# Optimization experiments

Hardware: AMD Instinct MI355X
Metric: run time of the kernel (lower is better)

Reference implementation:

```python
import jax, jax.numpy as jnp
import numpy as np

GAMMA = 2.0                  # n2n_gamma
WAVELET_WEIGHT = 0.05
THRESHOLD = 50.0 / 255.0     # wavelet_threshold normalized
LEVELS = 3


def conv_model(x, weight):
    # Stand-in denoising network: 1->1 channel 3x3 SAME conv.
    return jax.lax.conv_general_dilated(
        x, weight, window_strides=(1, 1), padding='SAME',
        dimension_numbers=('NCHW', 'OIHW', 'NCHW'))


def generate_subimages_checkerboard(noisy):
    # 2x2 checkerboard: (even,even) and (odd,odd), bilinearly upsampled back
    # to (H, W). jax.image.resize 'linear' uses half-pixel centers, matching
    # torch F.interpolate(mode='bilinear', align_corners=False).
    B, C, H, W = noisy.shape  # H, W assumed even (512)
    p0 = noisy[:, :, 0::2, 0::2]
    p3 = noisy[:, :, 1::2, 1::2]
    g1 = jax.image.resize(p0, (B, C, H, W), method='linear')
    g2 = jax.image.resize(p3, (B, C, H, W), method='linear')
    return g1, g2


def haar_level(x):
    # One level of batched 2D Haar DWT on x: [B, H, W] (H, W even).
    a = x[:, 0::2, 0::2]
    b = x[:, 0::2, 1::2]
    c = x[:, 1::2, 0::2]
    d = x[:, 1::2, 1::2]
    ll = (a + b + c + d) * 0.5
    lh = (a - b + c - d) * 0.5  # horizontal detail
    hl = (a + b - c - d) * 0.5  # vertical detail
    hh = (a - b - c + d) * 0.5  # diagonal detail
    return ll, (lh, hl, hh)


def wavelet_sparsity_loss(pred):
    # pred: [B, C, H, W]; only channel 0 is used (as in the original).
    # L1(c, soft_threshold(c, t)) == mean(min(|c|, t)) since the target is
    # detached; pywt's coeffs[1] is the COARSEST detail level, with
    # threshold t/2^(level_idx-1) and weight 1/level_idx, so the finest
    # decomposition step j maps to level_idx = LEVELS - j + 1.
    x = pred[:, 0]  # [B, H, W]
    total = jnp.asarray(0.0, dtype=x.dtype)
    cur = x
    for j in range(1, LEVELS + 1):  # j=1 finest
        cur, (h, v, d) = haar_level(cur)
        level_idx = LEVELS - j + 1
        thr = THRESHOLD / (2.0 ** (level_idx - 1))
        w = 1.0 / level_idx
        lvl = (jnp.mean(jnp.minimum(jnp.abs(h), thr)) +
               jnp.mean(jnp.minimum(jnp.abs(v), thr)) +
               jnp.mean(jnp.minimum(jnp.abs(d), thr))) / 3.0
        total = total + w * lvl
    return total


def setup_inputs() -> dict:
    key = jax.random.key(0)
    k1, k2 = jax.random.split(key)
    noisy_input = jax.random.uniform(k1, (32, 1, 512, 512), dtype=jnp.float32)
    weight = jax.random.normal(k2, (1, 1, 3, 3), dtype=jnp.float32) * (1.0 / 3.0)
    return {"noisy_input": noisy_input, "weight": weight}


def reference(noisy_input, weight):
    g1, g2 = generate_subimages_checkerboard(noisy_input)
    out = jnp.clip(conv_model(g1, weight), 0.0, 1.0)
    rec = jnp.mean((out - g2) ** 2)
    reg = jnp.mean((out - g1) ** 2)
    n2n_total = rec + GAMMA * reg
    # Original detaches pred to numpy for the wavelet prior -> no gradient.
    wavelet = jax.lax.stop_gradient(wavelet_sparsity_loss(out))
    return n2n_total + WAVELET_WEIGHT * wavelet
```

## Files before the change

### kernel.cpp

```cpp
#include <hip/hip_runtime.h>

namespace {

constexpr int   IMG = 512;
constexpr float THR = 50.0f / 255.0f;
constexpr int   NBLOCKS = (IMG / 32) * (IMG / 32) * 32;

constexpr double N_PIX = 32.0 * 512.0 * 512.0;
constexpr double N_L1  = 32.0 * 256.0 * 256.0;
constexpr double N_L2  = 32.0 * 128.0 * 128.0;
constexpr double N_L3  = 32.0 * 64.0 * 64.0;
constexpr double C_REC = 1.0 / N_PIX;
constexpr double C_REG = 2.0 / N_PIX;
constexpr double C_W1  = 0.05 / (9.0 * N_L1);
constexpr double C_W2  = 0.05 / (6.0 * N_L2);
constexpr double C_W3  = 0.05 / (3.0 * N_L3);

__global__ __launch_bounds__(256) void n2n_wavelet_kernel(
    const float* __restrict__ noisy,
    const float* __restrict__ weight,
    double* __restrict__ partial) {
  __shared__ float sP0[18][20];
  __shared__ float sP3[18][20];
  __shared__ float sG1[34][36];
  __shared__ float sOut[32][36];
  __shared__ float sLL1[16][18];
  __shared__ float sLL2[8][10];
  __shared__ float sRed[4][5];

  const int t  = threadIdx.x;
  const int tx = blockIdx.x;
  const int ty = blockIdx.y;
  const int b  = blockIdx.z;
  const float* img = noisy + (size_t)b * IMG * IMG;

  const int py0 = 16 * ty - 1;
  const int px0 = 16 * tx - 1;

  float wk[9];
#pragma unroll
  for (int i = 0; i < 9; ++i) wk[i] = weight[i];

  {
    const int r = t >> 4, c = t & 15;
    auto stage = [&](int rr, int cc) {
      int gr = py0 + rr; gr = gr < 0 ? 0 : (gr > 255 ? 255 : gr);
      int gc = px0 + cc; gc = gc < 0 ? 0 : (gc > 255 ? 255 : gc);
      sP0[rr][cc] = img[(gr * 2) * IMG + gc * 2];
      sP3[rr][cc] = img[(gr * 2 + 1) * IMG + gc * 2 + 1];
    };
    stage(r, c);
    if (c < 2) stage(r, c + 16);
    if (r < 2) stage(r + 16, c);
    if (r < 2 && c < 2) stage(r + 16, c + 16);
  }
  __syncthreads();

  const int gyb0 = 32 * ty, gxb0 = 32 * tx;

  for (int q = t; q < 289; q += 256) {
    const int n = q / 17;
    const int m = q - n * 17;
    const float a  = sP0[n][m],     bb = sP0[n][m + 1];
    const float cc = sP0[n + 1][m], dd = sP0[n + 1][m + 1];
    const float xt0 = 0.75f * a + 0.25f * bb;
    const float xt1 = 0.25f * a + 0.75f * bb;
    const float xb0 = 0.75f * cc + 0.25f * dd;
    const float xb1 = 0.25f * cc + 0.75f * dd;
    float v00 = 0.75f * xt0 + 0.25f * xb0;
    float v01 = 0.75f * xt1 + 0.25f * xb1;
    float v10 = 0.25f * xt0 + 0.75f * xb0;
    float v11 = 0.25f * xt1 + 0.75f * xb1;
    const int gyt = gyb0 - 1 + 2 * n, gxl = gxb0 - 1 + 2 * m;
    const bool vt = (unsigned)gyt < (unsigned)IMG, vb = (unsigned)(gyt + 1) < (unsigned)IMG;
    const bool vl = (unsigned)gxl < (unsigned)IMG, vr = (unsigned)(gxl + 1) < (unsigned)IMG;
    v00 = (vt && vl) ? v00 : 0.0f;  v01 = (vt && vr) ? v01 : 0.0f;
    v10 = (vb && vl) ? v10 : 0.0f;  v11 = (vb && vr) ? v11 : 0.0f;
    *(float2*)&sG1[2 * n][2 * m]     = make_float2(v00, v01);
    *(float2*)&sG1[2 * n + 1][2 * m] = make_float2(v10, v11);
  }
  __syncthreads();

  float rec = 0.0f, rgg = 0.0f;
  {
    const int row  = t >> 3;
    const int col0 = (t & 7) << 2;
    float a0 = 0, a1 = 0, a2 = 0, a3 = 0;
    float g1c0 = 0, g1c1 = 0, g1c2 = 0, g1c3 = 0;
#pragma unroll
    for (int u = 0; u < 3; ++u) {
      const float4 q4 = *(const float4*)&sG1[row + u][col0];
      const float2 e2 = *(const float2*)&sG1[row + u][col0 + 4];
      const float w0 = wk[3 * u], w1 = wk[3 * u + 1], w2 = wk[3 * u + 2];
      a0 += w0 * q4.x + w1 * q4.y + w2 * q4.z;
      a1 += w0 * q4.y + w1 * q4.z + w2 * q4.w;
      a2 += w0 * q4.z + w1 * q4.w + w2 * e2.x;
      a3 += w0 * q4.w + w1 * e2.x + w2 * e2.y;
      if (u == 1) { g1c0 = q4.y; g1c1 = q4.z; g1c2 = q4.w; g1c3 = e2.x; }
    }
    const float o0 = fminf(fmaxf(a0, 0.0f), 1.0f);
    const float o1 = fminf(fmaxf(a1, 0.0f), 1.0f);
    const float o2 = fminf(fmaxf(a2, 0.0f), 1.0f);
    const float o3 = fminf(fmaxf(a3, 0.0f), 1.0f);
    *(float4*)&sOut[row][col0] = make_float4(o0, o1, o2, o3);

    const int   r0l = (row >> 1) + (row & 1);
    const float wyt = (row & 1) ? 0.75f : 0.25f;
    const float wyb = 1.0f - wyt;
    const int   c0l = col0 >> 1;
    const float2 t01 = *(const float2*)&sP3[r0l][c0l];
    const float2 t23 = *(const float2*)&sP3[r0l][c0l + 2];
    const float2 b01 = *(const float2*)&sP3[r0l + 1][c0l];
    const float2 b23 = *(const float2*)&sP3[r0l + 1][c0l + 2];
    const float xt0 = 0.25f * t01.x + 0.75f * t01.y;
    const float xt1 = 0.75f * t01.y + 0.25f * t23.x;
    const float xt2 = 0.25f * t01.y + 0.75f * t23.x;
    const float xt3 = 0.75f * t23.x + 0.25f * t23.y;
    const float xb0 = 0.25f * b01.x + 0.75f * b01.y;
    const float xb1 = 0.75f * b01.y + 0.25f * b23.x;
    const float xb2 = 0.25f * b01.y + 0.75f * b23.x;
    const float xb3 = 0.75f * b23.x + 0.25f * b23.y;
    const float g20 = wyt * xt0 + wyb * xb0;
    const float g21 = wyt * xt1 + wyb * xb1;
    const float g22 = wyt * xt2 + wyb * xb2;
    const float g23 = wyt * xt3 + wyb * xb3;

    float d;
    d = o0 - g20; rec += d * d;   d = o1 - g21; rec += d * d;
    d = o2 - g22; rec += d * d;   d = o3 - g23; rec += d * d;
    d = o0 - g1c0; rgg += d * d;  d = o1 - g1c1; rgg += d * d;
    d = o2 - g1c2; rgg += d * d;  d = o3 - g1c3; rgg += d * d;
  }
  __syncthreads();

  float w1a = 0.0f, w2a = 0.0f, w3a = 0.0f;
  {
    const int i = t >> 4, j = t & 15;
    const float2 top = *(const float2*)&sOut[2 * i][2 * j];
    const float2 bot = *(const float2*)&sOut[2 * i + 1][2 * j];
    const float aa = top.x, bb = top.y, cc = bot.x, dd = bot.y;
    sLL1[i][j] = (aa + bb + cc + dd) * 0.5f;
    const float lh = (aa - bb + cc - dd) * 0.5f;
    const float hl = (aa + bb - cc - dd) * 0.5f;
    const float hh = (aa - bb - cc + dd) * 0.5f;
    const float th = THR * 0.25f;
    w1a = fminf(fabsf(lh), th) + fminf(fabsf(hl), th) + fminf(fabsf(hh), th);
  }
  __syncthreads();
  if (t < 64) {
    const int i = t >> 3, j = t & 7;
    const float2 top = *(const float2*)&sLL1[2 * i][2 * j];
    const float2 bot = *(const float2*)&sLL1[2 * i + 1][2 * j];
    const float aa = top.x, bb = top.y, cc = bot.x, dd = bot.y;
    sLL2[i][j] = (aa + bb + cc + dd) * 0.5f;
    const float lh = (aa - bb + cc - dd) * 0.5f;
    const float hl = (aa + bb - cc - dd) * 0.5f;
    const float hh = (aa - bb - cc + dd) * 0.5f;
    const float th = THR * 0.5f;
    w2a = fminf(fabsf(lh), th) + fminf(fabsf(hl), th) + fminf(fabsf(hh), th);
  }
  __syncthreads();
  if (t < 16) {
    const int i = t >> 2, j = t & 3;
    const float2 top = *(const float2*)&sLL2[2 * i][2 * j];
    const float2 bot = *(const float2*)&sLL2[2 * i + 1][2 * j];
    const float aa = top.x, bb = top.y, cc = bot.x, dd = bot.y;
    const float lh = (aa - bb + cc - dd) * 0.5f;
    const float hl = (aa + bb - cc - dd) * 0.5f;
    const float hh = (aa - bb - cc + dd) * 0.5f;
    w3a = fminf(fabsf(lh), THR) + fminf(fabsf(hl), THR) + fminf(fabsf(hh), THR);
  }

  float vals[5] = {rec, rgg, w1a, w2a, w3a};
#pragma unroll
  for (int v = 0; v < 5; ++v) {
    float x = vals[v];
#pragma unroll
    for (int off = 32; off > 0; off >>= 1) x += __shfl_down(x, off);
    vals[v] = x;
  }
  const int wave = t >> 6, lane = t & 63;
  if (lane == 0) {
#pragma unroll
    for (int v = 0; v < 5; ++v) sRed[wave][v] = vals[v];
  }
  __syncthreads();
  if (t == 0) {
    double s[5];
#pragma unroll
    for (int v = 0; v < 5; ++v)
      s[v] = (double)(sRed[0][v] + sRed[1][v] + sRed[2][v] + sRed[3][v]);
    const double contrib =
        C_REC * s[0] + C_REG * s[1] + C_W1 * s[2] + C_W2 * s[3] + C_W3 * s[4];
    const int bid = (blockIdx.z * gridDim.y + blockIdx.y) * gridDim.x + blockIdx.x;
    partial[bid] = contrib;
  }
}

__global__ __launch_bounds__(256) void finalize_kernel(
    const double* __restrict__ partial, float* __restrict__ out) {
  __shared__ double sRed[4];
  const int t = threadIdx.x;
  double s = 0.0;
  for (int i = t; i < NBLOCKS; i += 256) s += partial[i];
#pragma unroll
  for (int off = 32; off > 0; off >>= 1) s += __shfl_down(s, off);
  if ((t & 63) == 0) sRed[t >> 6] = s;
  __syncthreads();
  if (t == 0) out[0] = (float)(sRed[0] + sRed[1] + sRed[2] + sRed[3]);
}

}

extern "C" void kernel_launch(void* const* d_in, const int* in_sizes, int n_in,
                              void* d_out, int out_size, void* d_ws, size_t ws_size,
                              hipStream_t stream) {
  const float* noisy  = (const float*)d_in[0];
  const float* weight = (const float*)d_in[1];
  double* partial = (double*)d_ws;
  float* out = (float*)d_out;

  dim3 grid(IMG / 32, IMG / 32, 32);
  hipLaunchKernelGGL(n2n_wavelet_kernel, grid, dim3(256), 0, stream, noisy, weight, partial);
  hipLaunchKernelGGL(finalize_kernel, dim3(1), dim3(256), 0, stream, partial, out);
}
```

Measured before the change: 104.2 us.

## Replace shared-memory tiles with per-wave register strip pipeline and shuffles

Each wave now processes an 8-row strip across the full 512-pixel width, with each lane handling 8 columns. Upsampling, conv, loss terms and all three Haar levels are computed in registers, with neighbours exchanged by lane shuffles. This removes the shared-memory staging, the block barriers and the redundant halo loads of the 32x32 tile scheme, and reads rows as coalesced float4 loads. The cost is higher register pressure (launch bounds of 2 blocks per SM), fully unrolled code, and more partials (one per wave) for the finalize kernel to sum.

```diff
diff --git a/kernel.cpp b/kernel.cpp
--- a/kernel.cpp
+++ b/kernel.cpp
@@ -2,9 +2,12 @@
 
 namespace {
 
-constexpr int   IMG = 512;
+constexpr int IMG = 512;
+constexpr int S = 8;
+constexpr int NSTRIPS = IMG / S;
+constexpr int NWAVES = 32 * NSTRIPS;
+constexpr int NBLK = NWAVES / 4;
 constexpr float THR = 50.0f / 255.0f;
-constexpr int   NBLOCKS = (IMG / 32) * (IMG / 32) * 32;
 
 constexpr double N_PIX = 32.0 * 512.0 * 512.0;
 constexpr double N_L1  = 32.0 * 256.0 * 256.0;
@@ -16,184 +19,201 @@
 constexpr double C_W2  = 0.05 / (6.0 * N_L2);
 constexpr double C_W3  = 0.05 / (3.0 * N_L3);
 
-__global__ __launch_bounds__(256) void n2n_wavelet_kernel(
+struct F4 { float v[4]; };
+struct F8 { float v[8]; };
+struct Row { F8 g; float gl, gr; };
+
+__device__ __forceinline__ F4 load_even_cols(const float* rowp) {
+  const float4 lo = *(const float4*)rowp;
+  const float4 hi = *(const float4*)(rowp + 4);
+  F4 r; r.v[0] = lo.x; r.v[1] = lo.z; r.v[2] = hi.x; r.v[3] = hi.z; return r;
+}
+__device__ __forceinline__ F4 load_odd_cols(const float* rowp) {
+  const float4 lo = *(const float4*)rowp;
+  const float4 hi = *(const float4*)(rowp + 4);
+  F4 r; r.v[0] = lo.y; r.v[1] = lo.w; r.v[2] = hi.y; r.v[3] = hi.w; return r;
+}
+
+__device__ __forceinline__ F8 hblend(const F4& p, int lane) {
+  float left  = __shfl_up(p.v[3], 1);
+  float right = __shfl_down(p.v[0], 1);
+  if (lane == 0)  left  = p.v[0];
+  if (lane == 63) right = p.v[3];
+  F8 h;
+  h.v[0] = 0.25f*left   + 0.75f*p.v[0];
+  h.v[1] = 0.75f*p.v[0] + 0.25f*p.v[1];
+  h.v[2] = 0.25f*p.v[0] + 0.75f*p.v[1];
+  h.v[3] = 0.75f*p.v[1] + 0.25f*p.v[2];
+  h.v[4] = 0.25f*p.v[1] + 0.75f*p.v[2];
+  h.v[5] = 0.75f*p.v[2] + 0.25f*p.v[3];
+  h.v[6] = 0.25f*p.v[2] + 0.75f*p.v[3];
+  h.v[7] = 0.75f*p.v[3] + 0.25f*right;
+  return h;
+}
+
+__device__ __forceinline__ Row vblend(const F8& a, const F8& b, float wa, float wb, int lane) {
+  Row r;
+#pragma unroll
+  for (int c = 0; c < 8; ++c) r.g.v[c] = wa*a.v[c] + wb*b.v[c];
+  const float gl = __shfl_up(r.g.v[7], 1);
+  const float gr = __shfl_down(r.g.v[0], 1);
+  r.gl = (lane == 0)  ? 0.0f : gl;
+  r.gr = (lane == 63) ? 0.0f : gr;
+  return r;
+}
+
+__device__ __forceinline__ void conv_acc(const Row& r, const float* wk3, F8& acc) {
+#pragma unroll
+  for (int c = 0; c < 8; ++c) {
+    const float gm1 = (c == 0) ? r.gl : r.g.v[c-1];
+    const float gp1 = (c == 7) ? r.gr : r.g.v[c+1];
+    acc.v[c] += wk3[0]*gm1 + wk3[1]*r.g.v[c] + wk3[2]*gp1;
+  }
+}
+
+__device__ __forceinline__ F8 conv3(const Row& r0, const Row& r1, const Row& r2,
+                                    const float* wk) {
+  F8 o;
+#pragma unroll
+  for (int c = 0; c < 8; ++c) o.v[c] = 0.0f;
+  conv_acc(r0, wk + 0, o);
+  conv_acc(r1, wk + 3, o);
+  conv_acc(r2, wk + 6, o);
+#pragma unroll
+  for (int c = 0; c < 8; ++c) o.v[c] = fminf(fmaxf(o.v[c], 0.0f), 1.0f);
+  return o;
+}
+
+__device__ __forceinline__ F4 haarL1(const F8& e, const F8& o, float thr, float& acc) {
+  F4 ll;
+#pragma unroll
+  for (int c = 0; c < 4; ++c) {
+    const float a = e.v[2*c], b = e.v[2*c+1], cc = o.v[2*c], d = o.v[2*c+1];
+    ll.v[c] = (a + b + cc + d) * 0.5f;
+    const float lh = (a - b + cc - d) * 0.5f;
+    const float hl = (a + b - cc - d) * 0.5f;
+    const float hh = (a - b - cc + d) * 0.5f;
+    acc += fminf(fabsf(lh), thr) + fminf(fabsf(hl), thr) + fminf(fabsf(hh), thr);
+  }
+  return ll;
+}
+
+__device__ __forceinline__ float haar1pair(float a, float b, float cc, float d,
+                                           float thr, float& acc) {
+  const float lh = (a - b + cc - d) * 0.5f;
+  const float hl = (a + b - cc - d) * 0.5f;
+  const float hh = (a - b - cc + d) * 0.5f;
+  acc += fminf(fabsf(lh), thr) + fminf(fabsf(hl), thr) + fminf(fabsf(hh), thr);
+  return (a + b + cc + d) * 0.5f;
+}
+
+__global__ __launch_bounds__(256, 2) void n2n_wavelet_kernel(
     const float* __restrict__ noisy,
     const float* __restrict__ weight,
     double* __restrict__ partial) {
-  __shared__ float sP0[18][20];
-  __shared__ float sP3[18][20];
-  __shared__ float sG1[34][36];
-  __shared__ float sOut[32][36];
-  __shared__ float sLL1[16][18];
-  __shared__ float sLL2[8][10];
-  __shared__ float sRed[4][5];
-
-  const int t  = threadIdx.x;
-  const int tx = blockIdx.x;
-  const int ty = blockIdx.y;
-  const int b  = blockIdx.z;
-  const float* img = noisy + (size_t)b * IMG * IMG;
-
-  const int py0 = 16 * ty - 1;
-  const int px0 = 16 * tx - 1;
+  const int t = threadIdx.x;
+  const int lane = t & 63;
+  const int gwid = blockIdx.x * 4 + (t >> 6);
+  const int strip = gwid & (NSTRIPS - 1);
+  const int b = gwid >> 6;
+  const float* base = noisy + (size_t)b * IMG * IMG + lane * 8;
+
+  const int y0 = strip * S;
+  const int k0 = y0 >> 1;
+  const bool lastStrip = (y0 == IMG - S);
 
   float wk[9];
 #pragma unroll
   for (int i = 0; i < 9; ++i) wk[i] = weight[i];
 
-  {
-    const int r = t >> 4, c = t & 15;
-    auto stage = [&](int rr, int cc) {
-      int gr = py0 + rr; gr = gr < 0 ? 0 : (gr > 255 ? 255 : gr);
-      int gc = px0 + cc; gc = gc < 0 ? 0 : (gc > 255 ? 255 : gc);
-      sP0[rr][cc] = img[(gr * 2) * IMG + gc * 2];
-      sP3[rr][cc] = img[(gr * 2 + 1) * IMG + gc * 2 + 1];
-    };
-    stage(r, c);
-    if (c < 2) stage(r, c + 16);
-    if (r < 2) stage(r + 16, c);
-    if (r < 2 && c < 2) stage(r + 16, c + 16);
-  }
-  __syncthreads();
-
-  const int gyb0 = 32 * ty, gxb0 = 32 * tx;
-
-  for (int q = t; q < 289; q += 256) {
-    const int n = q / 17;
-    const int m = q - n * 17;
-    const float a  = sP0[n][m],     bb = sP0[n][m + 1];
-    const float cc = sP0[n + 1][m], dd = sP0[n + 1][m + 1];
-    const float xt0 = 0.75f * a + 0.25f * bb;
-    const float xt1 = 0.25f * a + 0.75f * bb;
-    const float xb0 = 0.75f * cc + 0.25f * dd;
-    const float xb1 = 0.25f * cc + 0.75f * dd;
-    float v00 = 0.75f * xt0 + 0.25f * xb0;
-    float v01 = 0.75f * xt1 + 0.25f * xb1;
-    float v10 = 0.25f * xt0 + 0.75f * xb0;
-    float v11 = 0.25f * xt1 + 0.75f * xb1;
-    const int gyt = gyb0 - 1 + 2 * n, gxl = gxb0 - 1 + 2 * m;
-    const bool vt = (unsigned)gyt < (unsigned)IMG, vb = (unsigned)(gyt + 1) < (unsigned)IMG;
-    const bool vl = (unsigned)gxl < (unsigned)IMG, vr = (unsigned)(gxl + 1) < (unsigned)IMG;
-    v00 = (vt && vl) ? v00 : 0.0f;  v01 = (vt && vr) ? v01 : 0.0f;
-    v10 = (vb && vl) ? v10 : 0.0f;  v11 = (vb && vr) ? v11 : 0.0f;
-    *(float2*)&sG1[2 * n][2 * m]     = make_float2(v00, v01);
-    *(float2*)&sG1[2 * n + 1][2 * m] = make_float2(v10, v11);
-  }
-  __syncthreads();
-
-  float rec = 0.0f, rgg = 0.0f;
-  {
-    const int row  = t >> 3;
-    const int col0 = (t & 7) << 2;
-    float a0 = 0, a1 = 0, a2 = 0, a3 = 0;
-    float g1c0 = 0, g1c1 = 0, g1c2 = 0, g1c3 = 0;
-#pragma unroll
-    for (int u = 0; u < 3; ++u) {
-      const float4 q4 = *(const float4*)&sG1[row + u][col0];
-      const float2 e2 = *(const float2*)&sG1[row + u][col0 + 4];
-      const float w0 = wk[3 * u], w1 = wk[3 * u + 1], w2 = wk[3 * u + 2];
-      a0 += w0 * q4.x + w1 * q4.y + w2 * q4.z;
-      a1 += w0 * q4.y + w1 * q4.z + w2 * q4.w;
-      a2 += w0 * q4.z + w1 * q4.w + w2 * e2.x;
-      a3 += w0 * q4.w + w1 * e2.x + w2 * e2.y;
-      if (u == 1) { g1c0 = q4.y; g1c1 = q4.z; g1c2 = q4.w; g1c3 = e2.x; }
-    }
-    const float o0 = fminf(fmaxf(a0, 0.0f), 1.0f);
-    const float o1 = fminf(fmaxf(a1, 0.0f), 1.0f);
-    const float o2 = fminf(fmaxf(a2, 0.0f), 1.0f);
-    const float o3 = fminf(fmaxf(a3, 0.0f), 1.0f);
-    *(float4*)&sOut[row][col0] = make_float4(o0, o1, o2, o3);
-
-    const int   r0l = (row >> 1) + (row & 1);
-    const float wyt = (row & 1) ? 0.75f : 0.25f;
-    const float wyb = 1.0f - wyt;
-    const int   c0l = col0 >> 1;
-    const float2 t01 = *(const float2*)&sP3[r0l][c0l];
-    const float2 t23 = *(const float2*)&sP3[r0l][c0l + 2];
-    const float2 b01 = *(const float2*)&sP3[r0l + 1][c0l];
-    const float2 b23 = *(const float2*)&sP3[r0l + 1][c0l + 2];
-    const float xt0 = 0.25f * t01.x + 0.75f * t01.y;
-    const float xt1 = 0.75f * t01.y + 0.25f * t23.x;
-    const float xt2 = 0.25f * t01.y + 0.75f * t23.x;
-    const float xt3 = 0.75f * t23.x + 0.25f * t23.y;
-    const float xb0 = 0.25f * b01.x + 0.75f * b01.y;
-    const float xb1 = 0.75f * b01.y + 0.25f * b23.x;
-    const float xb2 = 0.25f * b01.y + 0.75f * b23.x;
-    const float xb3 = 0.75f * b23.x + 0.25f * b23.y;
-    const float g20 = wyt * xt0 + wyb * xb0;
-    const float g21 = wyt * xt1 + wyb * xb1;
-    const float g22 = wyt * xt2 + wyb * xb2;
-    const float g23 = wyt * xt3 + wyb * xb3;
-
-    float d;
-    d = o0 - g20; rec += d * d;   d = o1 - g21; rec += d * d;
-    d = o2 - g22; rec += d * d;   d = o3 - g23; rec += d * d;
-    d = o0 - g1c0; rgg += d * d;  d = o1 - g1c1; rgg += d * d;
-    d = o2 - g1c2; rgg += d * d;  d = o3 - g1c3; rgg += d * d;
-  }
-  __syncthreads();
-
-  float w1a = 0.0f, w2a = 0.0f, w3a = 0.0f;
-  {
-    const int i = t >> 4, j = t & 15;
-    const float2 top = *(const float2*)&sOut[2 * i][2 * j];
-    const float2 bot = *(const float2*)&sOut[2 * i + 1][2 * j];
-    const float aa = top.x, bb = top.y, cc = bot.x, dd = bot.y;
-    sLL1[i][j] = (aa + bb + cc + dd) * 0.5f;
-    const float lh = (aa - bb + cc - dd) * 0.5f;
-    const float hl = (aa + bb - cc - dd) * 0.5f;
-    const float hh = (aa - bb - cc + dd) * 0.5f;
-    const float th = THR * 0.25f;
-    w1a = fminf(fabsf(lh), th) + fminf(fabsf(hl), th) + fminf(fabsf(hh), th);
-  }
-  __syncthreads();
-  if (t < 64) {
-    const int i = t >> 3, j = t & 7;
-    const float2 top = *(const float2*)&sLL1[2 * i][2 * j];
-    const float2 bot = *(const float2*)&sLL1[2 * i + 1][2 * j];
-    const float aa = top.x, bb = top.y, cc = bot.x, dd = bot.y;
-    sLL2[i][j] = (aa + bb + cc + dd) * 0.5f;
-    const float lh = (aa - bb + cc - dd) * 0.5f;
-    const float hl = (aa + bb - cc - dd) * 0.5f;
-    const float hh = (aa - bb - cc + dd) * 0.5f;
-    const float th = THR * 0.5f;
-    w2a = fminf(fabsf(lh), th) + fminf(fabsf(hl), th) + fminf(fabsf(hh), th);
-  }
-  __syncthreads();
-  if (t < 16) {
-    const int i = t >> 2, j = t & 3;
-    const float2 top = *(const float2*)&sLL2[2 * i][2 * j];
-    const float2 bot = *(const float2*)&sLL2[2 * i + 1][2 * j];
-    const float aa = top.x, bb = top.y, cc = bot.x, dd = bot.y;
-    const float lh = (aa - bb + cc - dd) * 0.5f;
-    const float hl = (aa + bb - cc - dd) * 0.5f;
-    const float hh = (aa - bb - cc + dd) * 0.5f;
-    w3a = fminf(fabsf(lh), THR) + fminf(fabsf(hl), THR) + fminf(fabsf(hh), THR);
+  float rec = 0.f, rgg = 0.f, w1a = 0.f, w2a = 0.f, w3a = 0.f;
+  const float thr1 = THR * 0.25f, thr2 = THR * 0.5f;
+
+  const int r0e = (k0 > 0) ? 2*(k0 - 1) : 0;
+  const F4 p0m = load_even_cols(base + r0e * IMG);
+  const F4 p0c = load_even_cols(base + (2*k0) * IMG);
+  const F4 p3m = load_odd_cols(base + (r0e + 1) * IMG);
+  const F4 p3c = load_odd_cols(base + (2*k0 + 1) * IMG);
+  const F8 hKm1 = hblend(p0m, lane);
+  F8 hCur  = hblend(p0c, lane);
+  F8 h3Prev = hblend(p3m, lane);
+  F8 h3Cur  = hblend(p3c, lane);
+
+  Row g1m, g1c;
+  if (y0 == 0) {
+#pragma unroll
+    for (int c = 0; c < 8; ++c) g1m.g.v[c] = 0.f;
+    g1m.gl = 0.f; g1m.gr = 0.f;
+  } else {
+    g1m = vblend(hKm1, hCur, 0.75f, 0.25f, lane);
+  }
+  g1c = vblend(hKm1, hCur, 0.25f, 0.75f, lane);
+
+  F4 ll1Prev;
+  float ll2Prev0 = 0.f, ll2Prev1 = 0.f;
+
+#pragma unroll
+  for (int p = 0; p < 4; ++p) {
+    const int k = k0 + p;
+    const int nr0 = (k < 255) ? 2*(k + 1) : 510;
+    const F4 p0n = load_even_cols(base + nr0 * IMG);
+    const F4 p3n = load_odd_cols(base + (nr0 + 1) * IMG);
+
+    const F8 hN = hblend(p0n, lane);
+    const Row g1p = vblend(hCur, hN, 0.75f, 0.25f, lane);
+
+    const F8 outE = conv3(g1m, g1c, g1p, wk);
+#pragma unroll
+    for (int c = 0; c < 8; ++c) {
+      const float g2 = 0.25f*h3Prev.v[c] + 0.75f*h3Cur.v[c];
+      float d = outE.v[c] - g2;        rec += d*d;
+      d = outE.v[c] - g1c.g.v[c];      rgg += d*d;
+    }
+
+    Row g1q = vblend(hCur, hN, 0.25f, 0.75f, lane);
+    if (lastStrip && p == 3) {
+#pragma unroll
+      for (int c = 0; c < 8; ++c) g1q.g.v[c] = 0.f;
+      g1q.gl = 0.f; g1q.gr = 0.f;
+    }
+    const F8 h3N = hblend(p3n, lane);
+
+    const F8 outO = conv3(g1c, g1p, g1q, wk);
+#pragma unroll
+    for (int c = 0; c < 8; ++c) {
+      const float g2 = 0.75f*h3Cur.v[c] + 0.25f*h3N.v[c];
+      float d = outO.v[c] - g2;        rec += d*d;
+      d = outO.v[c] - g1p.g.v[c];      rgg += d*d;
+    }
+
+    const F4 ll1 = haarL1(outE, outO, thr1, w1a);
+    if ((p & 1) == 0) {
+      ll1Prev = ll1;
+    } else {
+      const float ll20 = haar1pair(ll1Prev.v[0], ll1Prev.v[1], ll1.v[0], ll1.v[1], thr2, w2a);
+      const float ll21 = haar1pair(ll1Prev.v[2], ll1Prev.v[3], ll1.v[2], ll1.v[3], thr2, w2a);
+      if (p == 1) {
+        ll2Prev0 = ll20; ll2Prev1 = ll21;
+      } else {
+        const float lh = (ll2Prev0 - ll2Prev1 + ll20 - ll21) * 0.5f;
+        const float hl = (ll2Prev0 + ll2Prev1 - ll20 - ll21) * 0.5f;
+        const float hh = (ll2Prev0 - ll2Prev1 - ll20 + ll21) * 0.5f;
+        w3a += fminf(fabsf(lh), THR) + fminf(fabsf(hl), THR) + fminf(fabsf(hh), THR);
+      }
+    }
+
+    g1m = g1p; g1c = g1q; hCur = hN; h3Prev = h3Cur; h3Cur = h3N;
   }
 
   float vals[5] = {rec, rgg, w1a, w2a, w3a};
 #pragma unroll
   for (int v = 0; v < 5; ++v) {
-    float x = vals[v];
-#pragma unroll
-    for (int off = 32; off > 0; off >>= 1) x += __shfl_down(x, off);
-    vals[v] = x;
-  }
-  const int wave = t >> 6, lane = t & 63;
+#pragma unroll
+    for (int off = 32; off > 0; off >>= 1) vals[v] += __shfl_down(vals[v], off);
+  }
   if (lane == 0) {
-#pragma unroll
-    for (int v = 0; v < 5; ++v) sRed[wave][v] = vals[v];
-  }
-  __syncthreads();
-  if (t == 0) {
-    double s[5];
-#pragma unroll
-    for (int v = 0; v < 5; ++v)
-      s[v] = (double)(sRed[0][v] + sRed[1][v] + sRed[2][v] + sRed[3][v]);
-    const double contrib =
-        C_REC * s[0] + C_REG * s[1] + C_W1 * s[2] + C_W2 * s[3] + C_W3 * s[4];
-    const int bid = (blockIdx.z * gridDim.y + blockIdx.y) * gridDim.x + blockIdx.x;
-    partial[bid] = contrib;
+    partial[gwid] = C_REC*(double)vals[0] + C_REG*(double)vals[1]
+                  + C_W1*(double)vals[2] + C_W2*(double)vals[3] + C_W3*(double)vals[4];
   }
 }
 
@@ -202,7 +222,8 @@
   __shared__ double sRed[4];
   const int t = threadIdx.x;
   double s = 0.0;
-  for (int i = t; i < NBLOCKS; i += 256) s += partial[i];
+#pragma unroll
+  for (int i = 0; i < NWAVES / 256; ++i) s += partial[i * 256 + t];
 #pragma unroll
   for (int off = 32; off > 0; off >>= 1) s += __shfl_down(s, off);
   if ((t & 63) == 0) sRed[t >> 6] = s;
@@ -220,7 +241,7 @@
   double* partial = (double*)d_ws;
   float* out = (float*)d_out;
 
-  dim3 grid(IMG / 32, IMG / 32, 32);
-  hipLaunchKernelGGL(n2n_wavelet_kernel, grid, dim3(256), 0, stream, noisy, weight, partial);
+  hipLaunchKernelGGL(n2n_wavelet_kernel, dim3(NBLK), dim3(256), 0, stream,
+                     noisy, weight, partial);
   hipLaunchKernelGGL(finalize_kernel, dim3(1), dim3(256), 0, stream, partial, out);
 }
```

New measurement: 85.25 us. -18.2%, faster.
